# Performance work log

Measured on AMD Instinct MI355X. Metric: run time of the kernel, lower is better.

## Reference

```python
import jax, jax.numpy as jnp
import numpy as np

REND = 256
KPOOL = 7
SIGMA = 0.7  # soft-edge width in pixels for differentiable silhouette


def _sphere_mesh(n_lat=12, n_lon=16, radius=0.4):
    i = np.arange(n_lat); j = np.arange(n_lon)
    theta = np.pi * (i + 0.5) / n_lat
    phi = 2.0 * np.pi * j / n_lon
    T, P = np.meshgrid(theta, phi, indexing='ij')
    verts = np.stack([radius * np.sin(T) * np.cos(P),
                      radius * np.sin(T) * np.sin(P),
                      radius * np.cos(T)], -1).reshape(-1, 3)
    faces = []
    for a in range(n_lat - 1):
        for b in range(n_lon):
            b1 = (b + 1) % n_lon
            v00 = a * n_lon + b; v01 = a * n_lon + b1
            v10 = (a + 1) * n_lon + b; v11 = (a + 1) * n_lon + b1
            faces.append([v00, v10, v11]); faces.append([v00, v11, v01])
    return verts.astype(np.float32), np.asarray(faces, np.int32)


def setup_inputs() -> dict:
    key = jax.random.key(0)
    ks = jax.random.split(key, 8)
    B, H, W = 2, REND, REND
    verts_np, faces_np = _sphere_mesh()
    vertices = jnp.tile(jnp.asarray(verts_np)[None], (B, 1, 1))          # [B,V,3]
    faces = jnp.asarray(faces_np)                                        # [F,3]
    K = jnp.tile(jnp.array([[1.2, 0.0, 0.5], [0.0, 1.2, 0.5], [0.0, 0.0, 1.0]],
                           jnp.float32)[None], (B, 1, 1))                # [B,3,3]
    R = jnp.eye(3, dtype=jnp.float32)[None] + 0.05 * jax.random.normal(ks[0], (B, 3, 3), jnp.float32)
    obj_t = jnp.array([0.0, 0.0, 2.5], jnp.float32)[None] + 0.1 * jax.random.normal(ks[1], (B, 3), jnp.float32)
    obj_s = 0.8 + 0.4 * jax.random.uniform(ks[2], (B,), jnp.float32)
    keep_mask = (jax.random.uniform(ks[3], (B, H, W), jnp.float32) > 0.3).astype(jnp.float32)
    image_ref = (jax.random.uniform(ks[4], (B, H, W), jnp.float32) > 0.5).astype(jnp.float32)
    edt_ref_edge = jax.random.uniform(ks[5], (B, H, W), jnp.float32)
    return {"R": R, "obj_t": obj_t, "obj_s": obj_s, "vertices": vertices,
            "faces": faces, "K": K, "keep_mask": keep_mask,
            "image_ref": image_ref, "edt_ref_edge": edt_ref_edge}


def _silhouette(verts, faces, K, H, W, sigma=SIGMA):
    """Differentiable (soft) silhouette rasterizer: 1 - prod_f(1 - coverage_f)."""
    B = verts.shape[0]
    z = verts[..., 2]
    u = K[:, 0, 0, None] * verts[..., 0] / z + K[:, 0, 2, None]
    v = K[:, 1, 1, None] * verts[..., 1] / z + K[:, 1, 2, None]
    p2d = jnp.stack([u * W, v * H], -1)                   # [B,V,2] pixel coords (orig_size=1)
    tri = jnp.take(p2d, faces, axis=1)                    # [B,F,3,2]
    e01 = tri[:, :, 1] - tri[:, :, 0]
    e02 = tri[:, :, 2] - tri[:, :, 0]
    area2 = e01[..., 0] * e02[..., 1] - e01[..., 1] * e02[..., 0]   # [B,F]
    orient = jnp.where(area2 >= 0, 1.0, -1.0)
    px = jnp.arange(W, dtype=verts.dtype) + 0.5
    py = jnp.arange(H, dtype=verts.dtype) + 0.5
    Py, Px = jnp.meshgrid(py, px, indexing='ij')
    pxf = Px.reshape(-1); pyf = Py.reshape(-1)            # [P]
    P = pxf.shape[0]; F = faces.shape[0]
    prob = jnp.ones((B, P, F), verts.dtype)
    for k in range(3):  # 3 triangle edges (fixed small loop)
        a = tri[:, :, k]; b = tri[:, :, (k + 1) % 3]
        ex = b[..., 0] - a[..., 0]; ey = b[..., 1] - a[..., 1]          # [B,F]
        # signed edge distance of every pixel to edge (a->b)
        d = (ex[:, None, :] * (pyf[None, :, None] - a[..., 1][:, None, :])
             - ey[:, None, :] * (pxf[None, :, None] - a[..., 0][:, None, :]))
        inv = orient / (jnp.sqrt(ex * ex + ey * ey) + 1e-8) / sigma    # [B,F]
        prob = prob * jax.nn.sigmoid(d * inv[:, None, :])
    prob = jnp.clip(prob, 0.0, 1.0 - 1e-4)
    sil = 1.0 - jnp.prod(1.0 - prob, axis=-1)             # soft union over faces, [B,P]
    return sil.reshape(B, H, W)


def _maxpool(x, k=KPOOL):
    # MaxPool2d(kernel=k, stride=1, padding=k//2) on [B,H,W]
    return jax.lax.reduce_window(x, -jnp.inf, jax.lax.max, (1, k, k), (1, 1, 1), 'SAME')


def reference(R, obj_t, obj_s, vertices, faces, K, keep_mask, image_ref, edt_ref_edge):
    # apply_transformation: bmm(vertices, R) + t, then scale
    verts = obj_s[:, None, None] * (jnp.einsum('bvi,bij->bvj', vertices, R) + obj_t[:, None, :])
    image = keep_mask * _silhouette(verts, faces, K, REND, REND)
    loss_mask = jnp.sum((image - image_ref) ** 2, axis=(1, 2)).mean()
    edges = _maxpool(image) - image
    return (loss_mask, image, edges, image_ref, edt_ref_edge)
```

## Files before the change

### kernel.cpp

```cpp
#include <hip/hip_runtime.h>
#include <math.h>

#define HH 256
#define WW 256
#define NF 352
#define NV 192
#define SIGMA_F 0.7f
#define CUT_S (-8.0f)

__global__ __launch_bounds__(1024, 8) void sil_tile_kernel(
    const float* __restrict__ Rm, const float* __restrict__ obj_t,
    const float* __restrict__ obj_s, const float* __restrict__ verts,
    const int* __restrict__ faces, const float* __restrict__ Km,
    const float* __restrict__ keep_mask, const float* __restrict__ image_ref,
    const float* __restrict__ edt_src,
    float* __restrict__ out_image, float* __restrict__ loss_partials,
    float* __restrict__ out_iref, float* __restrict__ out_edt)
{
    __shared__ float2 vxy[NV];
    __shared__ float4 coA[NF];
    __shared__ float4 coB[NF];
    __shared__ float  coC[NF];
    __shared__ unsigned short flist[4][NF];
    __shared__ int fcount[4];
    __shared__ float accB[3][4 * 64];
    __shared__ float wsum[4];

    const int tid  = threadIdx.x;
    const int lane = tid & 63;
    const int wv   = tid >> 6;
    const int grp  = wv >> 2;
    const int q    = wv & 3;
    const int blk  = blockIdx.x;
    const int b    = blk >> 8;
    const int t    = blk & 255;
    const int x0   = (t & 15) * 16, y0 = (t >> 4) * 16;
    const int sx   = (q & 1) * 8,  sy = (q >> 1) * 8;

    if (tid < NV) {
        const float* Rb = Rm + b * 9;
        const float s  = obj_s[b];
        const float t0 = obj_t[b*3+0], t1 = obj_t[b*3+1], t2 = obj_t[b*3+2];
        const float K00 = Km[b*9+0], K02 = Km[b*9+2], K11 = Km[b*9+4], K12 = Km[b*9+5];
        const float* vp = verts + (b * NV + tid) * 3;
        float v0 = vp[0], v1 = vp[1], v2 = vp[2];
        float w0 = s * (v0*Rb[0] + v1*Rb[3] + v2*Rb[6] + t0);
        float w1 = s * (v0*Rb[1] + v1*Rb[4] + v2*Rb[7] + t1);
        float w2 = s * (v0*Rb[2] + v1*Rb[5] + v2*Rb[8] + t2);
        float X = (K00 * w0 / w2 + K02) * (float)WW;
        float Y = (K11 * w1 / w2 + K12) * (float)HH;
        vxy[tid] = {X, Y};
    }
    __syncthreads();

    if (tid < NF) {
        const int f = tid;
        int i0 = faces[f*3+0], i1 = faces[f*3+1], i2 = faces[f*3+2];
        float2 P0 = vxy[i0], P1 = vxy[i1], P2 = vxy[i2];
        float X[3] = {P0.x, P1.x, P2.x};
        float Y[3] = {P0.y, P1.y, P2.y};
        float e01x = X[1]-X[0], e01y = Y[1]-Y[0];
        float e02x = X[2]-X[0], e02y = Y[2]-Y[0];
        float area2 = e01x*e02y - e01y*e02x;
        float orient = (area2 >= 0.0f) ? 1.0f : -1.0f;
        float E[9];
        #pragma unroll
        for (int k = 0; k < 3; ++k) {
            int k1 = (k == 2) ? 0 : k + 1;
            float ax = X[k], ay = Y[k];
            float ex = X[k1]-ax, ey = Y[k1]-ay;
            float inv = orient / (sqrtf(ex*ex + ey*ey) + 1e-8f) / SIGMA_F;
            E[k*3 + 0] = ex * inv;
            E[k*3 + 1] = -ey * inv;
            E[k*3 + 2] = inv * (ey*ax - ex*ay);
        }
        coA[f] = {E[0], E[1], E[2], E[3]};
        coB[f] = {E[4], E[5], E[6], E[7]};
        coC[f] = E[8];
    }
    __syncthreads();

    if (grp == 0) {
        const float pxc = (float)(x0 + sx) + 4.0f;
        const float pyc = (float)(y0 + sy) + 4.0f;
        int base = 0;
        #pragma unroll
        for (int r = 0; r < 6; ++r) {
            int f = r * 64 + lane;
            bool keepf = false;
            if (f < NF) {
                float4 a4 = coA[f]; float4 b4 = coB[f]; float c2 = coC[f];
                float m0 = fmaf(a4.x,pyc,fmaf(a4.y,pxc,a4.z)) + 4.0f*(fabsf(a4.x)+fabsf(a4.y));
                float m1 = fmaf(a4.w,pyc,fmaf(b4.x,pxc,b4.y)) + 4.0f*(fabsf(a4.w)+fabsf(b4.x));
                float m2 = fmaf(b4.z,pyc,fmaf(b4.w,pxc,c2 )) + 4.0f*(fabsf(b4.z)+fabsf(b4.w));
                keepf = fminf(m0, fminf(m1, m2)) > CUT_S;
            }
            unsigned long long m = __ballot(keepf);
            if (keepf) {
                int pre = __popcll(m & ((1ull << lane) - 1ull));
                flist[q][base + pre] = (unsigned short)f;
            }
            base += __popcll(m);
        }
        if (lane == 0) fcount[q] = base;
    }
    __syncthreads();

    const int n  = fcount[q];
    const int lo = (n * grp) >> 2;
    const int hi = (n * (grp + 1)) >> 2;
    const int lx = lane & 7, ly = lane >> 3;
    const float px = (float)(x0 + sx + lx) + 0.5f;
    const float py = (float)(y0 + sy + ly) + 0.5f;
    float acc = 1.0f;
    for (int i = lo; i < hi; ++i) {
        int idx = flist[q][i];
        float4 a4 = coA[idx]; float4 b4 = coB[idx]; float c2 = coC[idx];
        float s0 = fmaf(a4.x, py, fmaf(a4.y, px, a4.z));
        float s1 = fmaf(a4.w, py, fmaf(b4.x, px, b4.y));
        float s2 = fmaf(b4.z, py, fmaf(b4.w, px, c2));
        float e0 = __expf(-s0), e1 = __expf(-s1), e2 = __expf(-s2);
        float pr = __builtin_amdgcn_rcpf((1.0f+e0) * (1.0f+e1) * (1.0f+e2));
        pr = fminf(pr, 0.9999f);
        acc *= (1.0f - pr);
    }
    if (grp != 0) accB[grp - 1][q * 64 + lane] = acc;
    __syncthreads();

    float sq = 0.0f;
    if (grp == 0) {
        acc *= accB[0][q * 64 + lane];
        acc *= accB[1][q * 64 + lane];
        acc *= accB[2][q * 64 + lane];
        float sil = 1.0f - acc;
        const int gidx = b*HH*WW + (y0 + sy + ly)*WW + (x0 + sx + lx);
        float img = keep_mask[gidx] * sil;
        out_image[gidx] = img;
        float d = img - image_ref[gidx];
        sq = d * d;
    }

    if (tid < 512) {
        int g = blk * 256 + (tid & 255);
        if (tid < 256)      out_iref[g] = image_ref[g];
        else                out_edt[g]  = edt_src[g];
    }

    #pragma unroll
    for (int o = 32; o > 0; o >>= 1) sq += __shfl_down(sq, o);
    if (grp == 0 && lane == 0) wsum[q] = sq;
    __syncthreads();
    if (tid == 0) loss_partials[blk] = wsum[0] + wsum[1] + wsum[2] + wsum[3];
}

__global__ __launch_bounds__(256) void post_kernel(
    const float* __restrict__ image, const float* __restrict__ partials,
    float* __restrict__ out_loss, float* __restrict__ out_edges)
{
    __shared__ float tile[22][23];
    __shared__ float rmax[22][16];
    __shared__ float lsum[4];

    const int tid = threadIdx.x;
    const int b   = blockIdx.x >> 8;
    const int t   = blockIdx.x & 255;
    const int x0  = (t & 15) * 16, y0 = (t >> 4) * 16;
    const float* im = image + b * (HH*WW);

    for (int i = tid; i < 22*22; i += 256) {
        int r = i / 22, cidx = i % 22;
        int yy = y0 + r - 3, xx = x0 + cidx - 3;
        float v = -INFINITY;
        if (yy >= 0 && yy < HH && xx >= 0 && xx < WW) v = im[yy * WW + xx];
        tile[r][cidx] = v;
    }
    __syncthreads();

    for (int i = tid; i < 22*16; i += 256) {
        int r = i >> 4, c = i & 15;
        float m = tile[r][c];
        #pragma unroll
        for (int d = 1; d < 7; ++d) m = fmaxf(m, tile[r][c + d]);
        rmax[r][c] = m;
    }
    __syncthreads();

    const int lx = tid & 15, ly = tid >> 4;
    float m = rmax[ly][lx];
    #pragma unroll
    for (int d = 1; d < 7; ++d) m = fmaxf(m, rmax[ly + d][lx]);
    const int gidx = b * (HH*WW) + (y0 + ly) * WW + (x0 + lx);
    out_edges[gidx] = m - tile[ly + 3][lx + 3];

    if (blockIdx.x == 0) {
        float v = partials[tid] + partials[tid + 256];
        #pragma unroll
        for (int o = 32; o > 0; o >>= 1) v += __shfl_down(v, o);
        if ((tid & 63) == 0) lsum[tid >> 6] = v;
        __syncthreads();
        if (tid == 0)
            out_loss[0] = (lsum[0] + lsum[1] + lsum[2] + lsum[3]) * 0.5f;
    }
}

extern "C" void kernel_launch(void* const* d_in, const int* in_sizes, int n_in,
                              void* d_out, int out_size, void* d_ws, size_t ws_size,
                              hipStream_t stream) {
    const float* Rm    = (const float*)d_in[0];
    const float* obj_t = (const float*)d_in[1];
    const float* obj_s = (const float*)d_in[2];
    const float* verts = (const float*)d_in[3];
    const int*   faces = (const int*)d_in[4];
    const float* Km    = (const float*)d_in[5];
    const float* keep  = (const float*)d_in[6];
    const float* iref  = (const float*)d_in[7];
    const float* edt   = (const float*)d_in[8];

    float* out       = (float*)d_out;
    float* out_loss  = out;
    float* out_image = out + 1;
    float* out_edges = out + 1 + 131072;
    float* out_iref  = out + 1 + 262144;
    float* out_edt   = out + 1 + 393216;
    float* partials  = (float*)d_ws;

    sil_tile_kernel<<<512, 1024, 0, stream>>>(Rm, obj_t, obj_s, verts, faces, Km,
                                              keep, iref, edt,
                                              out_image, partials, out_iref, out_edt);
    post_kernel<<<512, 256, 0, stream>>>(out_image, partials, out_loss, out_edges);
}
```

Measured before the change: 16.85 us.

## Order strongly-covering faces first and exit early once silhouette saturates

```diff
diff --git a/kernel.cpp b/kernel.cpp
--- a/kernel.cpp
+++ b/kernel.cpp
@@ -7,6 +7,8 @@
 #define NV 192
 #define SIGMA_F 0.7f
 #define CUT_S (-8.0f)
+#define STRONG_S (10.0f)
+#define EXIT_T (1.0e-3f)
 
 __global__ __launch_bounds__(1024, 8) void sil_tile_kernel(
     const float* __restrict__ Rm, const float* __restrict__ obj_t,
@@ -87,13 +89,36 @@
         #pragma unroll
         for (int r = 0; r < 6; ++r) {
             int f = r * 64 + lane;
+            bool strong = false;
+            if (f < NF) {
+                float4 a4 = coA[f]; float4 b4 = coB[f]; float c2 = coC[f];
+                float n0 = fmaf(a4.x,pyc,fmaf(a4.y,pxc,a4.z)) - 4.0f*(fabsf(a4.x)+fabsf(a4.y));
+                float n1 = fmaf(a4.w,pyc,fmaf(b4.x,pxc,b4.y)) - 4.0f*(fabsf(a4.w)+fabsf(b4.x));
+                float n2 = fmaf(b4.z,pyc,fmaf(b4.w,pxc,c2 )) - 4.0f*(fabsf(b4.z)+fabsf(b4.w));
+                strong = fminf(n0, fminf(n1, n2)) >= STRONG_S;
+            }
+            unsigned long long m = __ballot(strong);
+            if (strong) {
+                int pre = __popcll(m & ((1ull << lane) - 1ull));
+                flist[q][base + pre] = (unsigned short)f;
+            }
+            base += __popcll(m);
+        }
+        #pragma unroll
+        for (int r = 0; r < 6; ++r) {
+            int f = r * 64 + lane;
             bool keepf = false;
             if (f < NF) {
                 float4 a4 = coA[f]; float4 b4 = coB[f]; float c2 = coC[f];
-                float m0 = fmaf(a4.x,pyc,fmaf(a4.y,pxc,a4.z)) + 4.0f*(fabsf(a4.x)+fabsf(a4.y));
-                float m1 = fmaf(a4.w,pyc,fmaf(b4.x,pxc,b4.y)) + 4.0f*(fabsf(a4.w)+fabsf(b4.x));
-                float m2 = fmaf(b4.z,pyc,fmaf(b4.w,pxc,c2 )) + 4.0f*(fabsf(b4.z)+fabsf(b4.w));
-                keepf = fminf(m0, fminf(m1, m2)) > CUT_S;
+                float ax_ = 4.0f*(fabsf(a4.x)+fabsf(a4.y));
+                float bx_ = 4.0f*(fabsf(a4.w)+fabsf(b4.x));
+                float cx_ = 4.0f*(fabsf(b4.z)+fabsf(b4.w));
+                float c0 = fmaf(a4.x,pyc,fmaf(a4.y,pxc,a4.z));
+                float c1 = fmaf(a4.w,pyc,fmaf(b4.x,pxc,b4.y));
+                float c2v= fmaf(b4.z,pyc,fmaf(b4.w,pxc,c2 ));
+                bool strong = fminf(c0-ax_, fminf(c1-bx_, c2v-cx_)) >= STRONG_S;
+                bool keep   = fminf(c0+ax_, fminf(c1+bx_, c2v+cx_)) >  CUT_S;
+                keepf = keep && !strong;
             }
             unsigned long long m = __ballot(keepf);
             if (keepf) {
@@ -107,13 +132,11 @@
     __syncthreads();
 
     const int n  = fcount[q];
-    const int lo = (n * grp) >> 2;
-    const int hi = (n * (grp + 1)) >> 2;
     const int lx = lane & 7, ly = lane >> 3;
     const float px = (float)(x0 + sx + lx) + 0.5f;
     const float py = (float)(y0 + sy + ly) + 0.5f;
     float acc = 1.0f;
-    for (int i = lo; i < hi; ++i) {
+    for (int i = grp; i < n; i += 4) {
         int idx = flist[q][i];
         float4 a4 = coA[idx]; float4 b4 = coB[idx]; float c2 = coC[idx];
         float s0 = fmaf(a4.x, py, fmaf(a4.y, px, a4.z));
@@ -123,6 +146,7 @@
         float pr = __builtin_amdgcn_rcpf((1.0f+e0) * (1.0f+e1) * (1.0f+e2));
         pr = fminf(pr, 0.9999f);
         acc *= (1.0f - pr);
+        if (__all(acc < EXIT_T)) break;
     }
     if (grp != 0) accB[grp - 1][q * 64 + lane] = acc;
     __syncthreads();
```

New measurement: 17.45 us. +3.6%, slower.
